# Performance work log

Measured on AMD Instinct MI355X. Metric: run time of the kernel, lower is better.

Reference implementation:

```python
import jax, jax.numpy as jnp
import numpy as np

BATCH = 16384
MAX_ACTIVE = 32
FEAT = 768
HIDDEN = 1024


def setup_inputs() -> dict:
    key = jax.random.key(0)
    k1, k2, k3, k4, k5, k6 = jax.random.split(key, 6)
    stm = jax.random.randint(k1, (BATCH, MAX_ACTIVE), 0, FEAT, dtype=jnp.int32)
    nstm = jax.random.randint(k2, (BATCH, MAX_ACTIVE), 0, FEAT, dtype=jnp.int32)
    # Linear params (PyTorch layout: weight is (out_features, in_features))
    ft_w = jax.random.normal(k3, (HIDDEN, FEAT), dtype=jnp.float32) * 0.05
    ft_b = jax.random.normal(k4, (HIDDEN,), dtype=jnp.float32) * 0.05
    out_w = jax.random.normal(k5, (1, 2 * HIDDEN), dtype=jnp.float32) * 0.05
    out_b = jax.random.normal(k6, (1,), dtype=jnp.float32) * 0.05
    return {"stm": stm, "nstm": nstm, "ft_w": ft_w, "ft_b": ft_b,
            "out_w": out_w, "out_b": out_b}


def sparse_to_dense(indices: jnp.ndarray, size: int = FEAT) -> jnp.ndarray:
    """(B, max_active) int indices with -1 padding -> (B, size) 0/1 float32."""
    b = indices.shape[0]
    valid = (indices >= 0).astype(jnp.float32)          # (B, A)
    cols = jnp.clip(indices, 0, size - 1)               # padded -> col 0, masked by `valid`
    rows = jnp.arange(b, dtype=jnp.int32)[:, None]      # (B, 1) broadcast
    dense = jnp.zeros((b, size), dtype=jnp.float32)
    # .max matches torch's set-to-1 semantics even if duplicate indices occur
    return dense.at[rows, cols].max(valid)


def reference(stm, nstm, ft_w, ft_b, out_w, out_b):
    stm_d = sparse_to_dense(stm)                        # (B, 768)
    nstm_d = sparse_to_dense(nstm)                      # (B, 768)
    stm_h = stm_d @ ft_w.T + ft_b                       # (B, H)
    nstm_h = nstm_d @ ft_w.T + ft_b                     # (B, H)
    hidden = jnp.concatenate([stm_h, nstm_h], axis=1)   # (B, 2H)
    hidden = jnp.clip(hidden, 0.0, 1.0)
    return jax.nn.sigmoid(hidden @ out_w.T + out_b)     # (B, 1)
```

## Files before the change

### kernel.cpp

```cpp
#include <hip/hip_runtime.h>
#include <hip/hip_bf16.h>
#include <stdint.h>

#define BATCH 16384
#define MAXA 32
#define FEAT 768
#define HIDDEN 1024

__global__ __launch_bounds__(256) void scale_k(const float* __restrict__ ftw,
                                               float* __restrict__ scale,
                                               float* __restrict__ invsc,
                                               uint8_t* __restrict__ wQ) {
  if (blockIdx.x == HIDDEN) {
    if (threadIdx.x < 64) {
      uint4 v; v.x = v.y = v.z = v.w = 0x80808080u;
      ((uint4*)(wQ + (size_t)FEAT * HIDDEN))[threadIdx.x] = v;
    }
    return;
  }
  const int h = blockIdx.x;
  float a = 0.f;
#pragma unroll
  for (int p = 0; p < 3; ++p)
    a = fmaxf(a, fabsf(ftw[h * FEAT + p * 256 + threadIdx.x]));
#pragma unroll
  for (int off = 32; off > 0; off >>= 1)
    a = fmaxf(a, __shfl_xor(a, off, 64));
  __shared__ float red[4];
  if ((threadIdx.x & 63) == 0) red[threadIdx.x >> 6] = a;
  __syncthreads();
  if (threadIdx.x == 0) {
    float m = fmaxf(fmaxf(red[0], red[1]), fmaxf(red[2], red[3]));
    m = fmaxf(m, 1e-20f);
    scale[h] = m / 127.f;
    invsc[h] = 127.f / m;
  }
}

__global__ __launch_bounds__(256) void tilequant(const float* __restrict__ ftw,
                                                 const float* __restrict__ invsc,
                                                 uint8_t* __restrict__ wQ) {
  const int f0 = (blockIdx.x % (FEAT / 64)) * 64;
  const int h0 = (blockIdx.x / (FEAT / 64)) * 64;
  __shared__ uint8_t tile[64][80];
  __shared__ float inv[64];
  if (threadIdx.x < 64) inv[threadIdx.x] = invsc[h0 + threadIdx.x];
  __syncthreads();
  const int ff = threadIdx.x & 63;
  const int hb = threadIdx.x >> 6;
#pragma unroll
  for (int p = 0; p < 16; ++p) {
    int hh = p * 4 + hb;
    float w = ftw[(size_t)(h0 + hh) * FEAT + f0 + ff];
    int q = __float2int_rn(w * inv[hh]);
    tile[ff][hh] = (uint8_t)(q + 128);
  }
  __syncthreads();
  const int fs = threadIdx.x >> 2, part = threadIdx.x & 3;
  uint4 v = *(const uint4*)&tile[fs][part * 16];
  *(uint4*)(wQ + (size_t)(f0 + fs) * HIDDEN + h0 + part * 16) = v;
}

__device__ __forceinline__ void acc16(uint32_t* acc, uint4 w) {
  acc[0] += __builtin_amdgcn_perm(0u, w.x, 0x0c010c00u);
  acc[1] += __builtin_amdgcn_perm(0u, w.x, 0x0c030c02u);
  acc[2] += __builtin_amdgcn_perm(0u, w.y, 0x0c010c00u);
  acc[3] += __builtin_amdgcn_perm(0u, w.y, 0x0c030c02u);
  acc[4] += __builtin_amdgcn_perm(0u, w.z, 0x0c010c00u);
  acc[5] += __builtin_amdgcn_perm(0u, w.z, 0x0c030c02u);
  acc[6] += __builtin_amdgcn_perm(0u, w.w, 0x0c010c00u);
  acc[7] += __builtin_amdgcn_perm(0u, w.w, 0x0c030c02u);
}

__global__ __launch_bounds__(256, 6) void nn_fwd(
    const int* __restrict__ stm, const int* __restrict__ nstm,
    const uint8_t* __restrict__ wQ, const float* __restrict__ scale,
    const float* __restrict__ bias, const float* __restrict__ outw,
    const float* __restrict__ outb, float* __restrict__ out)
{
  const int lane = threadIdx.x & 63;
  const int row  = blockIdx.x * 4 + (threadIdx.x >> 6);
  const int half = lane >> 5;
  const int pos  = lane & 31;

  const int* __restrict__ src = half ? nstm : stm;
  int idx = src[row * MAXA + pos];
  bool valid = idx >= 0;
#pragma unroll
  for (int j = 0; j < 31; ++j) {
    int other = __shfl(idx, (half << 5) | j, 64);
    if (j < pos && other == idx) valid = false;
  }
  int fmap = valid ? idx : FEAT;

#pragma unroll
  for (int k = 2; k <= 32; k <<= 1) {
#pragma unroll
    for (int j = k >> 1; j > 0; j >>= 1) {
      int other = __shfl_xor(fmap, j, 64);
      bool lower = (pos & j) == 0;
      bool desc  = (pos & k) != 0;
      int mn = min(fmap, other), mx = max(fmap, other);
      fmap = (lower != desc) ? mn : mx;
    }
  }

  uint32_t accs[8], accn[8];
#pragma unroll
  for (int k = 0; k < 8; ++k) { accs[k] = 0u; accn[k] = 0u; }

#pragma unroll
  for (int jb = 0; jb < 32; jb += 4) {
    uint4 ws[4], wn[4];
#pragma unroll
    for (int u = 0; u < 4; ++u) {
      int fs_ = __builtin_amdgcn_readlane(fmap, jb + u);
      int fn_ = __builtin_amdgcn_readlane(fmap, 32 + jb + u);
      ws[u] = ((const uint4*)(wQ + (size_t)fs_ * HIDDEN))[lane];
      wn[u] = ((const uint4*)(wQ + (size_t)fn_ * HIDDEN))[lane];
    }
#pragma unroll
    for (int u = 0; u < 4; ++u) { acc16(accs, ws[u]); acc16(accn, wn[u]); }
  }

  const int DB = 32 * 128;

  const int hbase = lane * 16;
  const float4* s4 = (const float4*)(scale + hbase);
  const float4* b4 = (const float4*)(bias + hbase);
  const float4* oS = (const float4*)(outw + hbase);
  const float4* oN = (const float4*)(outw + HIDDEN + hbase);
  float partial = 0.f;
#pragma unroll
  for (int q = 0; q < 4; ++q) {
    float4 sv = s4[q], bv = b4[q], ov = oS[q], nv = oN[q];
    const float* sp = &sv.x; const float* bp = &bv.x;
    const float* op = &ov.x; const float* np = &nv.x;
#pragma unroll
    for (int e = 0; e < 4; ++e) {
      int k = q * 4 + e;
      uint32_t as = accs[k >> 1], an = accn[k >> 1];
      int qs = (int)((k & 1) ? (as >> 16) : (as & 0xffffu)) - DB;
      int qn = (int)((k & 1) ? (an >> 16) : (an & 0xffffu)) - DB;
      float hs = fminf(fmaxf(fmaf((float)qs, sp[e], bp[e]), 0.f), 1.f);
      float hn = fminf(fmaxf(fmaf((float)qn, sp[e], bp[e]), 0.f), 1.f);
      partial += hs * op[e] + hn * np[e];
    }
  }
#pragma unroll
  for (int off = 32; off > 0; off >>= 1)
    partial += __shfl_down(partial, off, 64);
  if (lane == 0) {
    float y = partial + outb[0];
    out[row] = 1.f / (1.f + __expf(-y));
  }
}

extern "C" void kernel_launch(void* const* d_in, const int* in_sizes, int n_in,
                              void* d_out, int out_size, void* d_ws, size_t ws_size,
                              hipStream_t stream) {
  const int*   stm  = (const int*)d_in[0];
  const int*   nstm = (const int*)d_in[1];
  const float* ftw  = (const float*)d_in[2];
  const float* ftb  = (const float*)d_in[3];
  const float* outw = (const float*)d_in[4];
  const float* outb = (const float*)d_in[5];

  uint8_t* wQ    = (uint8_t*)d_ws;
  float*   scale = (float*)(wQ + (size_t)(FEAT + 1) * HIDDEN);
  float*   invsc = scale + HIDDEN;

  scale_k<<<HIDDEN + 1, 256, 0, stream>>>(ftw, scale, invsc, wQ);
  tilequant<<<(FEAT / 64) * (HIDDEN / 64), 256, 0, stream>>>(ftw, invsc, wQ);
  nn_fwd<<<BATCH / 4, 256, 0, stream>>>(stm, nstm, wQ, scale, ftb, outw, outb,
                                        (float*)d_out);
}
```

Before: 120.3 us.

## Deduplicate features across 16-row blocks and stage unique weight rows in LDS

Each 1024-thread block now handles 16 batch rows. It builds a shared bitmap of the active features in the block and compacts it into a list of unique features. Those unique quantized weight rows are fetched once into LDS in 64-row chunks, with the next chunk prefetched into registers. Each wave then accumulates from LDS using ballot and readlane to pick its own features. This removes redundant L2/global weight fetches across rows, at the cost of two block-wide barriers per chunk, 64KB of LDS that limits occupancy, and serial per-feature loops; the padding-row trick and the bitonic sort are dropped in favour of a per-row bias correction.

```diff
diff --git a/kernel.cpp b/kernel.cpp
--- a/kernel.cpp
+++ b/kernel.cpp
@@ -6,18 +6,12 @@
 #define MAXA 32
 #define FEAT 768
 #define HIDDEN 1024
+#define RPB 16
+#define CHUNK 64
 
 __global__ __launch_bounds__(256) void scale_k(const float* __restrict__ ftw,
                                                float* __restrict__ scale,
-                                               float* __restrict__ invsc,
-                                               uint8_t* __restrict__ wQ) {
-  if (blockIdx.x == HIDDEN) {
-    if (threadIdx.x < 64) {
-      uint4 v; v.x = v.y = v.z = v.w = 0x80808080u;
-      ((uint4*)(wQ + (size_t)FEAT * HIDDEN))[threadIdx.x] = v;
-    }
-    return;
-  }
+                                               float* __restrict__ invsc) {
   const int h = blockIdx.x;
   float a = 0.f;
 #pragma unroll
@@ -72,58 +66,114 @@
   acc[7] += __builtin_amdgcn_perm(0u, w.w, 0x0c030c02u);
 }
 
-__global__ __launch_bounds__(256, 6) void nn_fwd(
+__global__ __launch_bounds__(1024, 8) void nn_fwd(
     const int* __restrict__ stm, const int* __restrict__ nstm,
     const uint8_t* __restrict__ wQ, const float* __restrict__ scale,
     const float* __restrict__ bias, const float* __restrict__ outw,
     const float* __restrict__ outb, float* __restrict__ out)
 {
-  const int lane = threadIdx.x & 63;
-  const int row  = blockIdx.x * 4 + (threadIdx.x >> 6);
+  const int tid  = threadIdx.x;
+  const int lane = tid & 63;
+  const int w    = tid >> 6;
+  const int row  = blockIdx.x * RPB + w;
   const int half = lane >> 5;
   const int pos  = lane & 31;
 
+  __shared__ uint32_t bitmap[24];
+  __shared__ uint32_t wordbase[24];
+  __shared__ int      s_unique;
+  __shared__ uint16_t ulist[FEAT];
+  __shared__ uint4    buf[CHUNK * 64];
+
+  if (tid < 24) bitmap[tid] = 0u;
+  __syncthreads();
+
   const int* __restrict__ src = half ? nstm : stm;
-  int idx = src[row * MAXA + pos];
-  bool valid = idx >= 0;
+  int f = src[row * MAXA + pos];
+  bool valid = f >= 0;
 #pragma unroll
   for (int j = 0; j < 31; ++j) {
-    int other = __shfl(idx, (half << 5) | j, 64);
-    if (j < pos && other == idx) valid = false;
-  }
-  int fmap = valid ? idx : FEAT;
-
-#pragma unroll
-  for (int k = 2; k <= 32; k <<= 1) {
-#pragma unroll
-    for (int j = k >> 1; j > 0; j >>= 1) {
-      int other = __shfl_xor(fmap, j, 64);
-      bool lower = (pos & j) == 0;
-      bool desc  = (pos & k) != 0;
-      int mn = min(fmap, other), mx = max(fmap, other);
-      fmap = (lower != desc) ? mn : mx;
-    }
-  }
+    int other = __shfl(f, (half << 5) | j, 64);
+    if (j < pos && other == f) valid = false;
+  }
+  if (valid) atomicOr((unsigned int*)&bitmap[f >> 5], 1u << (f & 31));
+  __syncthreads();
+
+  if (tid < 64) {
+    uint32_t wv = (tid < 24) ? bitmap[tid] : 0u;
+    int cnt = __popc(wv);
+    int inc = cnt;
+#pragma unroll
+    for (int off = 1; off < 32; off <<= 1) {
+      int t = __shfl_up(inc, off, 64);
+      if (lane >= off) inc += t;
+    }
+    if (tid < 24) {
+      int excl = inc - cnt;
+      wordbase[tid] = (uint32_t)excl;
+      int r = excl; uint32_t wt = wv;
+      while (wt) { int b = __builtin_ctz(wt); wt &= wt - 1u;
+                   ulist[r++] = (uint16_t)(tid * 32 + b); }
+      if (tid == 23) s_unique = inc;
+    }
+  }
+  __syncthreads();
+
+  const int su = s_unique;
+  const int nchunks = (su + CHUNK - 1) / CHUNK;
+
+  int r_lane = 0x7FFFFFFF;
+  if (valid)
+    r_lane = (int)wordbase[f >> 5] +
+             __popc(bitmap[f >> 5] & ((1u << (f & 31)) - 1u));
+
+  const uint64_t vball = __ballot(valid);
+  const int DBs = 128 * (int)__popcll(vball & 0xffffffffull);
+  const int DBn = 128 * (int)__popcll(vball >> 32);
 
   uint32_t accs[8], accn[8];
 #pragma unroll
   for (int k = 0; k < 8; ++k) { accs[k] = 0u; accn[k] = 0u; }
 
-#pragma unroll
-  for (int jb = 0; jb < 32; jb += 4) {
-    uint4 ws[4], wn[4];
+  uint4 pf[4];
+#pragma unroll
+  for (int u = 0; u < 4; ++u) {
+    int rk = w * 4 + u;
+    if (rk < su) {
+      int ff = ulist[rk];
+      pf[u] = ((const uint4*)(wQ + (size_t)ff * HIDDEN))[lane];
+    }
+  }
+
+  for (int c = 0; c < nchunks; ++c) {
 #pragma unroll
     for (int u = 0; u < 4; ++u) {
-      int fs_ = __builtin_amdgcn_readlane(fmap, jb + u);
-      int fn_ = __builtin_amdgcn_readlane(fmap, 32 + jb + u);
-      ws[u] = ((const uint4*)(wQ + (size_t)fs_ * HIDDEN))[lane];
-      wn[u] = ((const uint4*)(wQ + (size_t)fn_ * HIDDEN))[lane];
-    }
-#pragma unroll
-    for (int u = 0; u < 4; ++u) { acc16(accs, ws[u]); acc16(accn, wn[u]); }
-  }
-
-  const int DB = 32 * 128;
+      int rk = c * CHUNK + w * 4 + u;
+      if (rk < su) buf[(w * 4 + u) * 64 + lane] = pf[u];
+    }
+    __syncthreads();
+#pragma unroll
+    for (int u = 0; u < 4; ++u) {
+      int rk = (c + 1) * CHUNK + w * 4 + u;
+      if (rk < su) {
+        int ff = ulist[rk];
+        pf[u] = ((const uint4*)(wQ + (size_t)ff * HIDDEN))[lane];
+      }
+    }
+    uint64_t inm = __ballot(valid && (unsigned)(r_lane - c * CHUNK) < CHUNK);
+    uint32_t ms = (uint32_t)inm, mn = (uint32_t)(inm >> 32);
+    while (ms) {
+      int j = __builtin_ctz(ms); ms &= ms - 1u;
+      int slot = __builtin_amdgcn_readlane(r_lane, j) - c * CHUNK;
+      acc16(accs, buf[slot * 64 + lane]);
+    }
+    while (mn) {
+      int j = __builtin_ctz(mn); mn &= mn - 1u;
+      int slot = __builtin_amdgcn_readlane(r_lane, 32 + j) - c * CHUNK;
+      acc16(accn, buf[slot * 64 + lane]);
+    }
+    __syncthreads();
+  }
 
   const int hbase = lane * 16;
   const float4* s4 = (const float4*)(scale + hbase);
@@ -140,8 +190,8 @@
     for (int e = 0; e < 4; ++e) {
       int k = q * 4 + e;
       uint32_t as = accs[k >> 1], an = accn[k >> 1];
-      int qs = (int)((k & 1) ? (as >> 16) : (as & 0xffffu)) - DB;
-      int qn = (int)((k & 1) ? (an >> 16) : (an & 0xffffu)) - DB;
+      int qs = (int)((k & 1) ? (as >> 16) : (as & 0xffffu)) - DBs;
+      int qn = (int)((k & 1) ? (an >> 16) : (an & 0xffffu)) - DBn;
       float hs = fminf(fmaxf(fmaf((float)qs, sp[e], bp[e]), 0.f), 1.f);
       float hn = fminf(fmaxf(fmaf((float)qn, sp[e], bp[e]), 0.f), 1.f);
       partial += hs * op[e] + hn * np[e];
@@ -167,11 +217,11 @@
   const float* outb = (const float*)d_in[5];
 
   uint8_t* wQ    = (uint8_t*)d_ws;
-  float*   scale = (float*)(wQ + (size_t)(FEAT + 1) * HIDDEN);
+  float*   scale = (float*)(wQ + (size_t)FEAT * HIDDEN);
   float*   invsc = scale + HIDDEN;
 
-  scale_k<<<HIDDEN + 1, 256, 0, stream>>>(ftw, scale, invsc, wQ);
+  scale_k<<<HIDDEN, 256, 0, stream>>>(ftw, scale, invsc);
   tilequant<<<(FEAT / 64) * (HIDDEN / 64), 256, 0, stream>>>(ftw, invsc, wQ);
-  nn_fwd<<<BATCH / 4, 256, 0, stream>>>(stm, nstm, wQ, scale, ftb, outw, outb,
-                                        (float*)d_out);
-}
+  nn_fwd<<<BATCH / RPB, 1024, 0, stream>>>(stm, nstm, wQ, scale, ftb, outw,
+                                           outb, (float*)d_out);
+}
```

New measurement: 265.6 us. 2.21x slower.

## Replicate quantized weight table per XCC and drop bitonic index sort

Applied to the files above, without the earlier changes.

The quantized weight table is written up to eight times into the workspace, and each block picks its copy using the hardware XCC id. The goal is to keep gathers local to each XCD's L2 and avoid cross-die traffic. The bitonic sort of active feature indices is also removed, which cuts shuffle work but loses sorted, locality-friendly access order. The extra copies add write traffic to the quantization kernels and need enough workspace.

```diff
diff --git a/kernel.cpp b/kernel.cpp
--- a/kernel.cpp
+++ b/kernel.cpp
@@ -6,15 +6,18 @@
 #define MAXA 32
 #define FEAT 768
 #define HIDDEN 1024
+#define REPSTRIDE ((size_t)(FEAT + 1) * HIDDEN)
 
 __global__ __launch_bounds__(256) void scale_k(const float* __restrict__ ftw,
                                                float* __restrict__ scale,
                                                float* __restrict__ invsc,
-                                               uint8_t* __restrict__ wQ) {
+                                               uint8_t* __restrict__ wQ,
+                                               int nrep) {
   if (blockIdx.x == HIDDEN) {
     if (threadIdx.x < 64) {
       uint4 v; v.x = v.y = v.z = v.w = 0x80808080u;
-      ((uint4*)(wQ + (size_t)FEAT * HIDDEN))[threadIdx.x] = v;
+      for (int r = 0; r < nrep; ++r)
+        ((uint4*)(wQ + r * REPSTRIDE + (size_t)FEAT * HIDDEN))[threadIdx.x] = v;
     }
     return;
   }
@@ -39,7 +42,8 @@
 
 __global__ __launch_bounds__(256) void tilequant(const float* __restrict__ ftw,
                                                  const float* __restrict__ invsc,
-                                                 uint8_t* __restrict__ wQ) {
+                                                 uint8_t* __restrict__ wQ,
+                                                 int nrep) {
   const int f0 = (blockIdx.x % (FEAT / 64)) * 64;
   const int h0 = (blockIdx.x / (FEAT / 64)) * 64;
   __shared__ uint8_t tile[64][80];
@@ -58,7 +62,9 @@
   __syncthreads();
   const int fs = threadIdx.x >> 2, part = threadIdx.x & 3;
   uint4 v = *(const uint4*)&tile[fs][part * 16];
-  *(uint4*)(wQ + (size_t)(f0 + fs) * HIDDEN + h0 + part * 16) = v;
+  size_t off = (size_t)(f0 + fs) * HIDDEN + h0 + part * 16;
+  for (int r = 0; r < nrep; ++r)
+    *(uint4*)(wQ + r * REPSTRIDE + off) = v;
 }
 
 __device__ __forceinline__ void acc16(uint32_t* acc, uint4 w) {
@@ -76,12 +82,16 @@
     const int* __restrict__ stm, const int* __restrict__ nstm,
     const uint8_t* __restrict__ wQ, const float* __restrict__ scale,
     const float* __restrict__ bias, const float* __restrict__ outw,
-    const float* __restrict__ outb, float* __restrict__ out)
+    const float* __restrict__ outb, float* __restrict__ out, int repmask)
 {
   const int lane = threadIdx.x & 63;
   const int row  = blockIdx.x * 4 + (threadIdx.x >> 6);
   const int half = lane >> 5;
   const int pos  = lane & 31;
+
+  uint32_t xcc;
+  asm("s_getreg_b32 %0, hwreg(HW_REG_XCC_ID)" : "=s"(xcc));
+  const uint8_t* __restrict__ wx = wQ + (size_t)(xcc & (uint32_t)repmask) * REPSTRIDE;
 
   const int* __restrict__ src = half ? nstm : stm;
   int idx = src[row * MAXA + pos];
@@ -91,19 +101,7 @@
     int other = __shfl(idx, (half << 5) | j, 64);
     if (j < pos && other == idx) valid = false;
   }
-  int fmap = valid ? idx : FEAT;
-
-#pragma unroll
-  for (int k = 2; k <= 32; k <<= 1) {
-#pragma unroll
-    for (int j = k >> 1; j > 0; j >>= 1) {
-      int other = __shfl_xor(fmap, j, 64);
-      bool lower = (pos & j) == 0;
-      bool desc  = (pos & k) != 0;
-      int mn = min(fmap, other), mx = max(fmap, other);
-      fmap = (lower != desc) ? mn : mx;
-    }
-  }
+  const int fmap = valid ? idx : FEAT;
 
   uint32_t accs[8], accn[8];
 #pragma unroll
@@ -116,8 +114,8 @@
     for (int u = 0; u < 4; ++u) {
       int fs_ = __builtin_amdgcn_readlane(fmap, jb + u);
       int fn_ = __builtin_amdgcn_readlane(fmap, 32 + jb + u);
-      ws[u] = ((const uint4*)(wQ + (size_t)fs_ * HIDDEN))[lane];
-      wn[u] = ((const uint4*)(wQ + (size_t)fn_ * HIDDEN))[lane];
+      ws[u] = ((const uint4*)(wx + (size_t)fs_ * HIDDEN))[lane];
+      wn[u] = ((const uint4*)(wx + (size_t)fn_ * HIDDEN))[lane];
     }
 #pragma unroll
     for (int u = 0; u < 4; ++u) { acc16(accs, ws[u]); acc16(accn, wn[u]); }
@@ -166,12 +164,17 @@
   const float* outw = (const float*)d_in[4];
   const float* outb = (const float*)d_in[5];
 
+  int nrep = 1;
+  while (nrep < 8 &&
+         (size_t)(nrep * 2) * REPSTRIDE + 2 * HIDDEN * sizeof(float) <= ws_size)
+    nrep *= 2;
+
   uint8_t* wQ    = (uint8_t*)d_ws;
-  float*   scale = (float*)(wQ + (size_t)(FEAT + 1) * HIDDEN);
+  float*   scale = (float*)(wQ + (size_t)nrep * REPSTRIDE);
   float*   invsc = scale + HIDDEN;
 
-  scale_k<<<HIDDEN + 1, 256, 0, stream>>>(ftw, scale, invsc, wQ);
-  tilequant<<<(FEAT / 64) * (HIDDEN / 64), 256, 0, stream>>>(ftw, invsc, wQ);
+  scale_k<<<HIDDEN + 1, 256, 0, stream>>>(ftw, scale, invsc, wQ, nrep);
+  tilequant<<<(FEAT / 64) * (HIDDEN / 64), 256, 0, stream>>>(ftw, invsc, wQ, nrep);
   nn_fwd<<<BATCH / 4, 256, 0, stream>>>(stm, nstm, wQ, scale, ftb, outw, outb,
-                                        (float*)d_out);
+                                        (float*)d_out, nrep - 1);
 }
```

After: 123.1 us. 2.3% more time.
